# Kernel tuning notes

Measured on AMD Instinct MI355X. Metric: run time of the kernel, lower is better.

Reference implementation:

```python
import jax, jax.numpy as jnp
import numpy as np

NUM_HEADS = 16

def setup_inputs() -> dict:
    key = jax.random.key(0)
    ks = jax.random.split(key, 5)
    B, T, C = 2, 2048, 1024
    s = 0.02
    return {
        "x": jax.random.normal(ks[0], (B, T, C), dtype=jnp.float32),
        "in_w": jax.random.normal(ks[1], (3 * C, C), dtype=jnp.float32) * s,
        "in_b": jax.random.normal(ks[2], (3 * C,), dtype=jnp.float32) * s,
        "out_w": jax.random.normal(ks[3], (C, C), dtype=jnp.float32) * s,
        "out_b": jax.random.normal(ks[4], (C,), dtype=jnp.float32) * s,
    }

def reference(x, in_w, in_b, out_w, out_b):
    B, T, C = x.shape
    H = NUM_HEADS
    D = C // H
    qvk = x @ in_w.T + in_b  # (B, T, 3C)
    # einops 'b t (d k h) -> k b h t d': factor 3C as (D, 3, H), D outermost
    qvk = qvk.reshape(B, T, D, 3, H).transpose(3, 0, 4, 1, 2)  # (3, B, H, T, D)
    q, v, k = qvk[0], qvk[1], qvk[2]  # note q, v, k assignment order
    scores = jnp.einsum('bhid,bhjd->bhij', q, k) * (D ** -0.5)  # (B, H, T, T)
    causal = jnp.tril(jnp.ones((T, T), dtype=bool))
    scores = jnp.where(causal, scores, -jnp.inf)
    attn = jax.nn.softmax(scores, axis=-1)
    out = jnp.einsum('bhij,bhjd->bhid', attn, v)  # (B, H, T, D)
    out = out.transpose(0, 2, 1, 3).reshape(B, T, C)  # 'b h t d -> b t (h d)'
    return out @ out_w.T + out_b
```

## Files before the change

### kernel.cpp

```cpp
#include <hip/hip_runtime.h>


#define BB 2
#define TT 2048
#define CC 1024
#define HH 16
#define DD 64
#define MM (BB*TT)
#define N3 (3*CC)
#define BH (BB*HH)

typedef unsigned short u16;
typedef unsigned int   u32;
typedef __bf16 bf16x8 __attribute__((ext_vector_type(8)));
typedef float  f32x4  __attribute__((ext_vector_type(4)));

__device__ __forceinline__ u16 f32_to_bf16(float f) {
  u32 u = __float_as_uint(f);
  return (u16)((u + 0x7fffu + ((u >> 16) & 1u)) >> 16);
}
__device__ __forceinline__ u16 f32_to_bf16_fast(float f) {
  return (u16)((__float_as_uint(f) + 0x8000u) >> 16);
}
__device__ __forceinline__ u32 pack2_bf16(float a, float b) {
  u32 ua = __float_as_uint(a) + 0x8000u;
  u32 ub = __float_as_uint(b) + 0x8000u;
  return __builtin_amdgcn_perm(ub, ua, 0x07060302);
}

__global__ __launch_bounds__(256) void cast_f32_bf16(const float* __restrict__ src,
                                                     u16* __restrict__ dst, int n4) {
  int i = blockIdx.x * 256 + threadIdx.x;
  if (i < n4) {
    float4 f = reinterpret_cast<const float4*>(src)[i];
    uint2 pk;
    pk.x = (u32)f32_to_bf16(f.x) | ((u32)f32_to_bf16(f.y) << 16);
    pk.y = (u32)f32_to_bf16(f.z) | ((u32)f32_to_bf16(f.w) << 16);
    reinterpret_cast<uint2*>(dst)[i] = pk;
  }
}

__device__ __forceinline__ void gemm_core(const u16* __restrict__ Ag,
                                          const u16* __restrict__ Bg,
                                          int K, u16* Al, u16* Bl,
                                          int m0, int n0, f32x4 acc[4][4]) {
  const int tid = threadIdx.x, lane = tid & 63, w = tid >> 6;
  const int quad = lane >> 4, colr = lane & 15;
  const int mw = (w >> 1) * 64, nw = (w & 1) * 64;
  const int srow = lane >> 3, scol = lane & 7;
  const uint4* Al4 = reinterpret_cast<const uint4*>(Al);
  const uint4* Bl4 = reinterpret_cast<const uint4*>(Bl);
  for (int kt = 0; kt < K / 64; ++kt) {
    __syncthreads();
    #pragma unroll
    for (int ii = 0; ii < 4; ++ii) {
      int inst = w * 4 + ii;
      int row = inst * 8 + srow;
      int cs = scol ^ (row & 7);
      const u16* ga = Ag + (size_t)(m0 + row) * K + kt * 64 + cs * 8;
      const u16* gb = Bg + (size_t)(n0 + row) * K + kt * 64 + cs * 8;
      __builtin_amdgcn_global_load_lds(
          (const __attribute__((address_space(1))) void*)ga,
          (__attribute__((address_space(3))) void*)(Al + inst * 512), 16, 0, 0);
      __builtin_amdgcn_global_load_lds(
          (const __attribute__((address_space(1))) void*)gb,
          (__attribute__((address_space(3))) void*)(Bl + inst * 512), 16, 0, 0);
    }
    __syncthreads();
    #pragma unroll
    for (int ks = 0; ks < 2; ++ks) {
      bf16x8 af[4], bfr[4];
      #pragma unroll
      for (int t = 0; t < 4; ++t) {
        int mrow = mw + t * 16 + colr;
        af[t]  = __builtin_bit_cast(bf16x8, Al4[mrow * 8 + ((ks * 4 + quad) ^ (mrow & 7))]);
        int nrow = nw + t * 16 + colr;
        bfr[t] = __builtin_bit_cast(bf16x8, Bl4[nrow * 8 + ((ks * 4 + quad) ^ (nrow & 7))]);
      }
      #pragma unroll
      for (int mt = 0; mt < 4; ++mt)
        #pragma unroll
        for (int nt = 0; nt < 4; ++nt)
          acc[mt][nt] = __builtin_amdgcn_mfma_f32_16x16x32_bf16(af[mt], bfr[nt], acc[mt][nt], 0, 0, 0);
    }
  }
}

__global__ __launch_bounds__(256) void gemm_qkv(const u16* __restrict__ xb,
                                                const u16* __restrict__ wb,
                                                const float* __restrict__ in_b,
                                                u16* __restrict__ Y) {
  __shared__ __align__(16) u16 Al[128 * 64];
  __shared__ __align__(16) u16 Bl[128 * 64];
  const int lane = threadIdx.x & 63, w = threadIdx.x >> 6;
  const int quad = lane >> 4, colr = lane & 15;
  const int mw = (w >> 1) * 64, nw = (w & 1) * 64;
  const int m0 = blockIdx.x * 128, n0 = blockIdx.y * 128;
  f32x4 acc[4][4];
  #pragma unroll
  for (int mt = 0; mt < 4; ++mt)
    #pragma unroll
    for (int nt = 0; nt < 4; ++nt) acc[mt][nt] = (f32x4){0.f, 0.f, 0.f, 0.f};
  gemm_core(xb, wb, CC, Al, Bl, m0, n0, acc);
  float bias[4];
  #pragma unroll
  for (int nt = 0; nt < 4; ++nt) bias[nt] = in_b[n0 + nw + nt * 16 + colr];
  #pragma unroll
  for (int mt = 0; mt < 4; ++mt)
    #pragma unroll
    for (int e = 0; e < 4; ++e) {
      int row = m0 + mw + mt * 16 + quad * 4 + e;
      #pragma unroll
      for (int nt = 0; nt < 4; ++nt)
        Y[(size_t)row * N3 + n0 + nw + nt * 16 + colr] = f32_to_bf16(acc[mt][nt][e] + bias[nt]);
    }
}

__global__ __launch_bounds__(256) void repack_qkv(const u16* __restrict__ Y,
                                                  u16* __restrict__ qkv) {
  __shared__ __align__(16) u16 Yl[N3];
  const int m = blockIdx.x, tid = threadIdx.x;
  const int b_ = m >> 11, t = m & (TT - 1);
  const uint4* Yg = reinterpret_cast<const uint4*>(Y + (size_t)m * N3);
  uint4* Yl4 = reinterpret_cast<uint4*>(Yl);
  for (int i = tid; i < N3 / 8; i += 256) Yl4[i] = Yg[i];
  __syncthreads();
  for (int it = tid; it < 768; it += 256) {
    int h = it & 15, s = (it >> 4) % 3, dg = it / 48;
    int col = s * 16 + h;
    u32 lo = (u32)Yl[(dg * 4 + 0) * 48 + col] | ((u32)Yl[(dg * 4 + 1) * 48 + col] << 16);
    u32 hi = (u32)Yl[(dg * 4 + 2) * 48 + col] | ((u32)Yl[(dg * 4 + 3) * 48 + col] << 16);
    uint2 pk; pk.x = lo; pk.y = hi;
    size_t base = (((size_t)s * BH + b_ * HH + h) * TT + t) * DD + dg * 4;
    *reinterpret_cast<uint2*>(qkv + base) = pk;
  }
}

__global__ __launch_bounds__(256) void attn_mfma(const u16* __restrict__ qkv,
                                                 u16* __restrict__ aout) {
  __shared__ __align__(16) u32   Vt[64 * 36];
  __shared__ __align__(16) float Pl[4 * 32 * 68];
  const int tid  = threadIdx.x;
  const int lane = tid & 63, w = tid >> 6;
  const int quad = lane >> 4, colr = lane & 15;
  const int flat = blockIdx.x;
  const int bh = (flat & 7) * 4 + (flat >> 6);
  const int pr = (flat >> 3) & 7;
  const int b_ = bh >> 4, h = bh & 15;

  const uint4* Qg4 = reinterpret_cast<const uint4*>(qkv + (size_t)bh * TT * DD);
  const uint4* Vg4 = reinterpret_cast<const uint4*>(qkv + ((size_t)BH + bh) * TT * DD);
  const uint4* Kg4 = reinterpret_cast<const uint4*>(qkv + ((size_t)2 * BH + bh) * TT * DD);
  const uint4*  Vt4 = reinterpret_cast<const uint4*>(Vt);
  const float4* Pl4 = reinterpret_cast<const float4*>(Pl);

  const int s_jp = tid & 31, s_oct = tid >> 5;
  const int wbase = w * (32 * 68);

  for (int pass = 0; pass < 2; ++pass) {
    const int qt = pass ? (15 - pr) : pr;
    const int i0 = qt * 128;
    const int jmax = 2 * qt + 1;

    bf16x8 qa[2][2];
    #pragma unroll
    for (int u = 0; u < 2; ++u)
      #pragma unroll
      for (int ks = 0; ks < 2; ++ks)
        qa[u][ks] = __builtin_bit_cast(bf16x8,
            Qg4[(size_t)(i0 + w * 32 + u * 16 + colr) * 8 + ks * 4 + quad]);

    f32x4 oacc[2][4];
    #pragma unroll
    for (int u = 0; u < 2; ++u)
      #pragma unroll
      for (int dt = 0; dt < 4; ++dt) oacc[u][dt] = (f32x4){0.f, 0.f, 0.f, 0.f};
    float lp[2] = {0.f, 0.f};

    uint4 va = Vg4[(size_t)(2 * s_jp) * 8 + s_oct];
    uint4 vb = Vg4[(size_t)(2 * s_jp + 1) * 8 + s_oct];

    for (int jt = 0; jt <= jmax; ++jt) {
      const int j0 = jt * 64;
      uint4 kraw[4][2];
      #pragma unroll
      for (int t4 = 0; t4 < 4; ++t4)
        #pragma unroll
        for (int ks = 0; ks < 2; ++ks)
          kraw[t4][ks] = Kg4[(size_t)(j0 + t4 * 16 + colr) * 8 + ks * 4 + quad];

      __syncthreads();
      {
        u32 aw[4] = {va.x, va.y, va.z, va.w};
        u32 bw[4] = {vb.x, vb.y, vb.z, vb.w};
        #pragma unroll
        for (int m = 0; m < 4; ++m) {
          Vt[(s_oct * 8 + 2 * m)     * 36 + s_jp] = __builtin_amdgcn_perm(bw[m], aw[m], 0x05040100);
          Vt[(s_oct * 8 + 2 * m + 1) * 36 + s_jp] = __builtin_amdgcn_perm(bw[m], aw[m], 0x07060302);
        }
      }
      __syncthreads();
      if (jt < jmax) {
        int nj = j0 + 64;
        va = Vg4[(size_t)(nj + 2 * s_jp) * 8 + s_oct];
        vb = Vg4[(size_t)(nj + 2 * s_jp + 1) * 8 + s_oct];
      }

      f32x4 sacc[2][4];
      #pragma unroll
      for (int u = 0; u < 2; ++u)
        #pragma unroll
        for (int t4 = 0; t4 < 4; ++t4) sacc[u][t4] = (f32x4){0.f, 0.f, 0.f, 0.f};
      #pragma unroll
      for (int t4 = 0; t4 < 4; ++t4)
        #pragma unroll
        for (int ks = 0; ks < 2; ++ks) {
          bf16x8 kb = __builtin_bit_cast(bf16x8, kraw[t4][ks]);
          #pragma unroll
          for (int u = 0; u < 2; ++u)
            sacc[u][t4] = __builtin_amdgcn_mfma_f32_16x16x32_bf16(qa[u][ks], kb, sacc[u][t4], 0, 0, 0);
        }

      const bool maskt = (jt >= 2 * qt);
      const int joff = (jt - 2 * qt) * 64;
      #pragma unroll
      for (int u = 0; u < 2; ++u)
        #pragma unroll
        for (int t4 = 0; t4 < 4; ++t4)
          #pragma unroll
          for (int rg = 0; rg < 4; ++rg) {
            float p = __builtin_amdgcn_exp2f(sacc[u][t4][rg] * 0.18033688011112042f);
            if (maskt && (joff + t4 * 16 + colr > w * 32 + u * 16 + quad * 4 + rg)) p = 0.f;
            Pl[wbase + (u * 16 + quad * 4 + rg) * 68 + t4 * 16 + colr] = p;
          }

      bf16x8 pa[2][2];
      #pragma unroll
      for (int u = 0; u < 2; ++u)
        #pragma unroll
        for (int ks = 0; ks < 2; ++ks) {
          int b4 = (wbase + (u * 16 + colr) * 68 + ks * 32 + quad * 8) >> 2;
          float4 f0 = Pl4[b4], f1 = Pl4[b4 + 1];
          lp[u] += ((f0.x + f0.y) + (f0.z + f0.w)) + ((f1.x + f1.y) + (f1.z + f1.w));
          uint4 up;
          up.x = pack2_bf16(f0.x, f0.y); up.y = pack2_bf16(f0.z, f0.w);
          up.z = pack2_bf16(f1.x, f1.y); up.w = pack2_bf16(f1.z, f1.w);
          pa[u][ks] = __builtin_bit_cast(bf16x8, up);
        }

      #pragma unroll
      for (int dt = 0; dt < 4; ++dt)
        #pragma unroll
        for (int ks = 0; ks < 2; ++ks) {
          bf16x8 vfr = __builtin_bit_cast(bf16x8, Vt4[(dt * 16 + colr) * 9 + ks * 4 + quad]);
          #pragma unroll
          for (int u = 0; u < 2; ++u)
            oacc[u][dt] = __builtin_amdgcn_mfma_f32_16x16x32_bf16(pa[u][ks], vfr, oacc[u][dt], 0, 0, 0);
        }
    }

    #pragma unroll
    for (int u = 0; u < 2; ++u) {
      float ls = lp[u];
      ls += __shfl_xor(ls, 16);
      ls += __shfl_xor(ls, 32);
      float linv[4];
      #pragma unroll
      for (int rg = 0; rg < 4; ++rg)
        linv[rg] = 1.0f / __shfl(ls, quad * 4 + rg);
      #pragma unroll
      for (int dt = 0; dt < 4; ++dt)
        #pragma unroll
        for (int rg = 0; rg < 4; ++rg) {
          int ig = i0 + w * 32 + u * 16 + quad * 4 + rg;
          size_t off = ((size_t)(b_ * TT + ig)) * CC + h * DD + dt * 16 + colr;
          aout[off] = f32_to_bf16_fast(oacc[u][dt][rg] * linv[rg]);
        }
    }
  }
}

__global__ __launch_bounds__(256) void gemm_out(const u16* __restrict__ ab,
                                                const u16* __restrict__ owb,
                                                const float* __restrict__ out_b,
                                                float* __restrict__ out) {
  __shared__ __align__(16) u16 Al[128 * 64];
  __shared__ __align__(16) u16 Bl[128 * 64];
  const int lane = threadIdx.x & 63, w = threadIdx.x >> 6;
  const int quad = lane >> 4, colr = lane & 15;
  const int mw = (w >> 1) * 64, nw = (w & 1) * 64;
  const int m0 = blockIdx.x * 128, n0 = blockIdx.y * 128;
  f32x4 acc[4][4];
  #pragma unroll
  for (int mt = 0; mt < 4; ++mt)
    #pragma unroll
    for (int nt = 0; nt < 4; ++nt) acc[mt][nt] = (f32x4){0.f, 0.f, 0.f, 0.f};
  gemm_core(ab, owb, CC, Al, Bl, m0, n0, acc);
  float bias[4];
  #pragma unroll
  for (int nt = 0; nt < 4; ++nt) bias[nt] = out_b[n0 + nw + nt * 16 + colr];
  #pragma unroll
  for (int mt = 0; mt < 4; ++mt)
    #pragma unroll
    for (int e = 0; e < 4; ++e) {
      int row = m0 + mw + mt * 16 + quad * 4 + e;
      #pragma unroll
      for (int nt = 0; nt < 4; ++nt)
        out[(size_t)row * CC + n0 + nw + nt * 16 + colr] = acc[mt][nt][e] + bias[nt];
    }
}

extern "C" void kernel_launch(void* const* d_in, const int* in_sizes, int n_in,
                              void* d_out, int out_size, void* d_ws, size_t ws_size,
                              hipStream_t stream) {
  const float* x     = (const float*)d_in[0];
  const float* in_w  = (const float*)d_in[1];
  const float* in_b  = (const float*)d_in[2];
  const float* out_w = (const float*)d_in[3];
  const float* out_b = (const float*)d_in[4];
  float* out = (float*)d_out;

  char* ws = (char*)d_ws;
  u16* xb  = (u16*)(ws + 0);
  u16* ab  = (u16*)(ws + 0);
  u16* wb  = (u16*)(ws + 8388608);
  u16* owb = (u16*)(ws + 14680064);
  u16* Y   = (u16*)(ws + 16777216);
  u16* qkv = (u16*)(ws + 41943040);

  cast_f32_bf16<<<dim3(MM * CC / 4 / 256), 256, 0, stream>>>(x, xb, MM * CC / 4);
  cast_f32_bf16<<<dim3(N3 * CC / 4 / 256), 256, 0, stream>>>(in_w, wb, N3 * CC / 4);
  cast_f32_bf16<<<dim3(CC * CC / 4 / 256), 256, 0, stream>>>(out_w, owb, CC * CC / 4);

  gemm_qkv<<<dim3(MM / 128, N3 / 128), 256, 0, stream>>>(xb, wb, in_b, Y);
  repack_qkv<<<dim3(MM), 256, 0, stream>>>(Y, qkv);
  attn_mfma<<<dim3(256), 256, 0, stream>>>(qkv, ab);
  gemm_out<<<dim3(MM / 128, CC / 128), 256, 0, stream>>>(ab, owb, out_b, out);
}
```

Before: 231.5 us.

## Split attention into one query tile per block with double-buffered V and fused casts

The attention kernel now launches 512 blocks, each handling a single 128-row query tile, ordered heaviest first. Before, 256 blocks each handled a paired short and long tile. The V transpose buffer is double-buffered so one barrier per key tile replaces two, and launch bounds request two blocks per CU. The three f32-to-bf16 cast launches are merged into one kernel that branches on index range. The aim is better CU occupancy and load balance and less launch and sync overhead, at the cost of more LDS per block and possible tail imbalance from unequal tile lengths.

```diff
diff --git a/kernel.cpp b/kernel.cpp
--- a/kernel.cpp
+++ b/kernel.cpp
@@ -28,16 +28,25 @@
   return __builtin_amdgcn_perm(ub, ua, 0x07060302);
 }
 
-__global__ __launch_bounds__(256) void cast_f32_bf16(const float* __restrict__ src,
-                                                     u16* __restrict__ dst, int n4) {
+#define N4_X  (MM * CC / 4)
+#define N4_W  (N3 * CC / 4)
+#define N4_OW (CC * CC / 4)
+__global__ __launch_bounds__(256) void cast_all(const float* __restrict__ x,
+                                                const float* __restrict__ in_w,
+                                                const float* __restrict__ out_w,
+                                                u16* __restrict__ xb,
+                                                u16* __restrict__ wb,
+                                                u16* __restrict__ owb) {
   int i = blockIdx.x * 256 + threadIdx.x;
-  if (i < n4) {
-    float4 f = reinterpret_cast<const float4*>(src)[i];
-    uint2 pk;
-    pk.x = (u32)f32_to_bf16(f.x) | ((u32)f32_to_bf16(f.y) << 16);
-    pk.y = (u32)f32_to_bf16(f.z) | ((u32)f32_to_bf16(f.w) << 16);
-    reinterpret_cast<uint2*>(dst)[i] = pk;
-  }
+  const float* src; u16* dst; int j;
+  if (i < N4_X)            { src = x;     dst = xb;  j = i; }
+  else if (i < N4_X + N4_W){ src = in_w;  dst = wb;  j = i - N4_X; }
+  else                     { src = out_w; dst = owb; j = i - N4_X - N4_W; }
+  float4 f = reinterpret_cast<const float4*>(src)[j];
+  uint2 pk;
+  pk.x = (u32)f32_to_bf16(f.x) | ((u32)f32_to_bf16(f.y) << 16);
+  pk.y = (u32)f32_to_bf16(f.z) | ((u32)f32_to_bf16(f.w) << 16);
+  reinterpret_cast<uint2*>(dst)[j] = pk;
 }
 
 __device__ __forceinline__ void gemm_core(const u16* __restrict__ Ag,
@@ -136,147 +145,144 @@
   }
 }
 
-__global__ __launch_bounds__(256) void attn_mfma(const u16* __restrict__ qkv,
-                                                 u16* __restrict__ aout) {
-  __shared__ __align__(16) u32   Vt[64 * 36];
+__global__ __launch_bounds__(256, 2) void attn_mfma(const u16* __restrict__ qkv,
+                                                    u16* __restrict__ aout) {
+  __shared__ __align__(16) u32   Vt[2][64 * 36];
   __shared__ __align__(16) float Pl[4 * 32 * 68];
   const int tid  = threadIdx.x;
   const int lane = tid & 63, w = tid >> 6;
   const int quad = lane >> 4, colr = lane & 15;
   const int flat = blockIdx.x;
-  const int bh = (flat & 7) * 4 + (flat >> 6);
-  const int pr = (flat >> 3) & 7;
+  const int bh = (flat & 7) * 4 + (flat >> 7);
+  const int qt = 15 - ((flat >> 3) & 15);
   const int b_ = bh >> 4, h = bh & 15;
+  const int i0 = qt * 128;
+  const int jmax = 2 * qt + 1;
 
   const uint4* Qg4 = reinterpret_cast<const uint4*>(qkv + (size_t)bh * TT * DD);
   const uint4* Vg4 = reinterpret_cast<const uint4*>(qkv + ((size_t)BH + bh) * TT * DD);
   const uint4* Kg4 = reinterpret_cast<const uint4*>(qkv + ((size_t)2 * BH + bh) * TT * DD);
-  const uint4*  Vt4 = reinterpret_cast<const uint4*>(Vt);
   const float4* Pl4 = reinterpret_cast<const float4*>(Pl);
 
   const int s_jp = tid & 31, s_oct = tid >> 5;
   const int wbase = w * (32 * 68);
 
-  for (int pass = 0; pass < 2; ++pass) {
-    const int qt = pass ? (15 - pr) : pr;
-    const int i0 = qt * 128;
-    const int jmax = 2 * qt + 1;
-
-    bf16x8 qa[2][2];
+  bf16x8 qa[2][2];
+  #pragma unroll
+  for (int u = 0; u < 2; ++u)
+    #pragma unroll
+    for (int ks = 0; ks < 2; ++ks)
+      qa[u][ks] = __builtin_bit_cast(bf16x8,
+          Qg4[(size_t)(i0 + w * 32 + u * 16 + colr) * 8 + ks * 4 + quad]);
+
+  f32x4 oacc[2][4];
+  #pragma unroll
+  for (int u = 0; u < 2; ++u)
+    #pragma unroll
+    for (int dt = 0; dt < 4; ++dt) oacc[u][dt] = (f32x4){0.f, 0.f, 0.f, 0.f};
+  float lp[2] = {0.f, 0.f};
+
+  uint4 va = Vg4[(size_t)(2 * s_jp) * 8 + s_oct];
+  uint4 vb = Vg4[(size_t)(2 * s_jp + 1) * 8 + s_oct];
+
+  for (int jt = 0; jt <= jmax; ++jt) {
+    const int j0 = jt * 64;
+    u32* vtw = Vt[jt & 1];
+    const uint4* vt4 = reinterpret_cast<const uint4*>(Vt[jt & 1]);
+
+    uint4 kraw[4][2];
+    #pragma unroll
+    for (int t4 = 0; t4 < 4; ++t4)
+      #pragma unroll
+      for (int ks = 0; ks < 2; ++ks)
+        kraw[t4][ks] = Kg4[(size_t)(j0 + t4 * 16 + colr) * 8 + ks * 4 + quad];
+
+    {
+      u32 aw[4] = {va.x, va.y, va.z, va.w};
+      u32 bw[4] = {vb.x, vb.y, vb.z, vb.w};
+      #pragma unroll
+      for (int m = 0; m < 4; ++m) {
+        vtw[(s_oct * 8 + 2 * m)     * 36 + s_jp] = __builtin_amdgcn_perm(bw[m], aw[m], 0x05040100);
+        vtw[(s_oct * 8 + 2 * m + 1) * 36 + s_jp] = __builtin_amdgcn_perm(bw[m], aw[m], 0x07060302);
+      }
+    }
+    if (jt < jmax) {
+      int nj = j0 + 64;
+      va = Vg4[(size_t)(nj + 2 * s_jp) * 8 + s_oct];
+      vb = Vg4[(size_t)(nj + 2 * s_jp + 1) * 8 + s_oct];
+    }
+    __syncthreads();
+
+    f32x4 sacc[2][4];
     #pragma unroll
     for (int u = 0; u < 2; ++u)
       #pragma unroll
-      for (int ks = 0; ks < 2; ++ks)
-        qa[u][ks] = __builtin_bit_cast(bf16x8,
-            Qg4[(size_t)(i0 + w * 32 + u * 16 + colr) * 8 + ks * 4 + quad]);
-
-    f32x4 oacc[2][4];
+      for (int t4 = 0; t4 < 4; ++t4) sacc[u][t4] = (f32x4){0.f, 0.f, 0.f, 0.f};
+    #pragma unroll
+    for (int t4 = 0; t4 < 4; ++t4)
+      #pragma unroll
+      for (int ks = 0; ks < 2; ++ks) {
+        bf16x8 kb = __builtin_bit_cast(bf16x8, kraw[t4][ks]);
+        #pragma unroll
+        for (int u = 0; u < 2; ++u)
+          sacc[u][t4] = __builtin_amdgcn_mfma_f32_16x16x32_bf16(qa[u][ks], kb, sacc[u][t4], 0, 0, 0);
+      }
+
+    const bool maskt = (jt >= 2 * qt);
+    const int joff = (jt - 2 * qt) * 64;
     #pragma unroll
     for (int u = 0; u < 2; ++u)
-      #pragma unroll
-      for (int dt = 0; dt < 4; ++dt) oacc[u][dt] = (f32x4){0.f, 0.f, 0.f, 0.f};
-    float lp[2] = {0.f, 0.f};
-
-    uint4 va = Vg4[(size_t)(2 * s_jp) * 8 + s_oct];
-    uint4 vb = Vg4[(size_t)(2 * s_jp + 1) * 8 + s_oct];
-
-    for (int jt = 0; jt <= jmax; ++jt) {
-      const int j0 = jt * 64;
-      uint4 kraw[4][2];
       #pragma unroll
       for (int t4 = 0; t4 < 4; ++t4)
         #pragma unroll
-        for (int ks = 0; ks < 2; ++ks)
-          kraw[t4][ks] = Kg4[(size_t)(j0 + t4 * 16 + colr) * 8 + ks * 4 + quad];
-
-      __syncthreads();
-      {
-        u32 aw[4] = {va.x, va.y, va.z, va.w};
-        u32 bw[4] = {vb.x, vb.y, vb.z, vb.w};
+        for (int rg = 0; rg < 4; ++rg) {
+          float p = __builtin_amdgcn_exp2f(sacc[u][t4][rg] * 0.18033688011112042f);
+          if (maskt && (joff + t4 * 16 + colr > w * 32 + u * 16 + quad * 4 + rg)) p = 0.f;
+          Pl[wbase + (u * 16 + quad * 4 + rg) * 68 + t4 * 16 + colr] = p;
+        }
+
+    bf16x8 pa[2][2];
+    #pragma unroll
+    for (int u = 0; u < 2; ++u)
+      #pragma unroll
+      for (int ks = 0; ks < 2; ++ks) {
+        int b4 = (wbase + (u * 16 + colr) * 68 + ks * 32 + quad * 8) >> 2;
+        float4 f0 = Pl4[b4], f1 = Pl4[b4 + 1];
+        lp[u] += ((f0.x + f0.y) + (f0.z + f0.w)) + ((f1.x + f1.y) + (f1.z + f1.w));
+        uint4 up;
+        up.x = pack2_bf16(f0.x, f0.y); up.y = pack2_bf16(f0.z, f0.w);
+        up.z = pack2_bf16(f1.x, f1.y); up.w = pack2_bf16(f1.z, f1.w);
+        pa[u][ks] = __builtin_bit_cast(bf16x8, up);
+      }
+
+    #pragma unroll
+    for (int dt = 0; dt < 4; ++dt)
+      #pragma unroll
+      for (int ks = 0; ks < 2; ++ks) {
+        bf16x8 vfr = __builtin_bit_cast(bf16x8, vt4[(dt * 16 + colr) * 9 + ks * 4 + quad]);
         #pragma unroll
-        for (int m = 0; m < 4; ++m) {
-          Vt[(s_oct * 8 + 2 * m)     * 36 + s_jp] = __builtin_amdgcn_perm(bw[m], aw[m], 0x05040100);
-          Vt[(s_oct * 8 + 2 * m + 1) * 36 + s_jp] = __builtin_amdgcn_perm(bw[m], aw[m], 0x07060302);
-        }
-      }
-      __syncthreads();
-      if (jt < jmax) {
-        int nj = j0 + 64;
-        va = Vg4[(size_t)(nj + 2 * s_jp) * 8 + s_oct];
-        vb = Vg4[(size_t)(nj + 2 * s_jp + 1) * 8 + s_oct];
-      }
-
-      f32x4 sacc[2][4];
-      #pragma unroll
-      for (int u = 0; u < 2; ++u)
-        #pragma unroll
-        for (int t4 = 0; t4 < 4; ++t4) sacc[u][t4] = (f32x4){0.f, 0.f, 0.f, 0.f};
-      #pragma unroll
-      for (int t4 = 0; t4 < 4; ++t4)
-        #pragma unroll
-        for (int ks = 0; ks < 2; ++ks) {
-          bf16x8 kb = __builtin_bit_cast(bf16x8, kraw[t4][ks]);
-          #pragma unroll
-          for (int u = 0; u < 2; ++u)
-            sacc[u][t4] = __builtin_amdgcn_mfma_f32_16x16x32_bf16(qa[u][ks], kb, sacc[u][t4], 0, 0, 0);
-        }
-
-      const bool maskt = (jt >= 2 * qt);
-      const int joff = (jt - 2 * qt) * 64;
-      #pragma unroll
-      for (int u = 0; u < 2; ++u)
-        #pragma unroll
-        for (int t4 = 0; t4 < 4; ++t4)
-          #pragma unroll
-          for (int rg = 0; rg < 4; ++rg) {
-            float p = __builtin_amdgcn_exp2f(sacc[u][t4][rg] * 0.18033688011112042f);
-            if (maskt && (joff + t4 * 16 + colr > w * 32 + u * 16 + quad * 4 + rg)) p = 0.f;
-            Pl[wbase + (u * 16 + quad * 4 + rg) * 68 + t4 * 16 + colr] = p;
-          }
-
-      bf16x8 pa[2][2];
-      #pragma unroll
-      for (int u = 0; u < 2; ++u)
-        #pragma unroll
-        for (int ks = 0; ks < 2; ++ks) {
-          int b4 = (wbase + (u * 16 + colr) * 68 + ks * 32 + quad * 8) >> 2;
-          float4 f0 = Pl4[b4], f1 = Pl4[b4 + 1];
-          lp[u] += ((f0.x + f0.y) + (f0.z + f0.w)) + ((f1.x + f1.y) + (f1.z + f1.w));
-          uint4 up;
-          up.x = pack2_bf16(f0.x, f0.y); up.y = pack2_bf16(f0.z, f0.w);
-          up.z = pack2_bf16(f1.x, f1.y); up.w = pack2_bf16(f1.z, f1.w);
-          pa[u][ks] = __builtin_bit_cast(bf16x8, up);
-        }
-
-      #pragma unroll
-      for (int dt = 0; dt < 4; ++dt)
-        #pragma unroll
-        for (int ks = 0; ks < 2; ++ks) {
-          bf16x8 vfr = __builtin_bit_cast(bf16x8, Vt4[(dt * 16 + colr) * 9 + ks * 4 + quad]);
-          #pragma unroll
-          for (int u = 0; u < 2; ++u)
-            oacc[u][dt] = __builtin_amdgcn_mfma_f32_16x16x32_bf16(pa[u][ks], vfr, oacc[u][dt], 0, 0, 0);
-        }
-    }
-
-    #pragma unroll
-    for (int u = 0; u < 2; ++u) {
-      float ls = lp[u];
-      ls += __shfl_xor(ls, 16);
-      ls += __shfl_xor(ls, 32);
-      float linv[4];
-      #pragma unroll
-      for (int rg = 0; rg < 4; ++rg)
-        linv[rg] = 1.0f / __shfl(ls, quad * 4 + rg);
-      #pragma unroll
-      for (int dt = 0; dt < 4; ++dt)
-        #pragma unroll
-        for (int rg = 0; rg < 4; ++rg) {
-          int ig = i0 + w * 32 + u * 16 + quad * 4 + rg;
-          size_t off = ((size_t)(b_ * TT + ig)) * CC + h * DD + dt * 16 + colr;
-          aout[off] = f32_to_bf16_fast(oacc[u][dt][rg] * linv[rg]);
-        }
-    }
+        for (int u = 0; u < 2; ++u)
+          oacc[u][dt] = __builtin_amdgcn_mfma_f32_16x16x32_bf16(pa[u][ks], vfr, oacc[u][dt], 0, 0, 0);
+      }
+  }
+
+  #pragma unroll
+  for (int u = 0; u < 2; ++u) {
+    float ls = lp[u];
+    ls += __shfl_xor(ls, 16);
+    ls += __shfl_xor(ls, 32);
+    float linv[4];
+    #pragma unroll
+    for (int rg = 0; rg < 4; ++rg)
+      linv[rg] = 1.0f / __shfl(ls, quad * 4 + rg);
+    #pragma unroll
+    for (int dt = 0; dt < 4; ++dt)
+      #pragma unroll
+      for (int rg = 0; rg < 4; ++rg) {
+        int ig = i0 + w * 32 + u * 16 + quad * 4 + rg;
+        size_t off = ((size_t)(b_ * TT + ig)) * CC + h * DD + dt * 16 + colr;
+        aout[off] = f32_to_bf16_fast(oacc[u][dt][rg] * linv[rg]);
+      }
   }
 }
 
@@ -328,12 +334,10 @@
   u16* Y   = (u16*)(ws + 16777216);
   u16* qkv = (u16*)(ws + 41943040);
 
-  cast_f32_bf16<<<dim3(MM * CC / 4 / 256), 256, 0, stream>>>(x, xb, MM * CC / 4);
-  cast_f32_bf16<<<dim3(N3 * CC / 4 / 256), 256, 0, stream>>>(in_w, wb, N3 * CC / 4);
-  cast_f32_bf16<<<dim3(CC * CC / 4 / 256), 256, 0, stream>>>(out_w, owb, CC * CC / 4);
+  cast_all<<<dim3((N4_X + N4_W + N4_OW) / 256), 256, 0, stream>>>(x, in_w, out_w, xb, wb, owb);
 
   gemm_qkv<<<dim3(MM / 128, N3 / 128), 256, 0, stream>>>(xb, wb, in_b, Y);
   repack_qkv<<<dim3(MM), 256, 0, stream>>>(Y, qkv);
-  attn_mfma<<<dim3(256), 256, 0, stream>>>(qkv, ab);
+  attn_mfma<<<dim3(512), 256, 0, stream>>>(qkv, ab);
   gemm_out<<<dim3(MM / 128, CC / 128), 256, 0, stream>>>(ab, owb, out_b, out);
 }
```

Result: slower. 250.3 us (+8.1%).
